# Kernel tuning notes

Hardware: AMD Instinct MI355X
Metric: run time of the kernel (lower is better)

Reference implementation:

```python
import jax, jax.numpy as jnp
import numpy as np

# pywt db4 reconstruction low-pass filter (rec_lo); this is exactly what the
# torch module stores in self.weights (initial_scaling_filter).
DB4_REC_LO = np.array([0.23037781330885523, 0.7148465705525415,
                       0.6308807679295904, -0.02798376941698385,
                       -0.18703481171888114, 0.030841381835986965,
                       0.032883011666982945, -0.010597401784997278],
                      dtype=np.float32)

B, N = 512, 65536  # batch, signal length


def setup_inputs() -> dict:
    key = jax.random.key(0)
    k1, k2, k3 = jax.random.split(key, 3)
    x1 = jax.random.normal(k1, (B, N), dtype=jnp.float32)        # signals
    x2 = jax.random.normal(k2, (B, 1, 8), dtype=jnp.float32)     # coeff placeholder (unused at layer 1)
    x3 = jax.random.normal(k3, (B, 1, 8), dtype=jnp.float32)     # reconstructions placeholder (pass-through)
    weights = jnp.asarray(DB4_REC_LO)                            # rec_lo, the module's Parameter
    return {"x1": x1, "x2": x2, "x3": x3, "weights": weights}


def _dwt_symmetric(x, rec_lo):
    """Batched pywt.dwt(x, 'db4', mode='symmetric'). x: (B, N) -> cA, cD: (B, (N+L-1)//2)."""
    L = rec_lo.shape[0]
    # pywt orthogonal-wavelet filter relations
    dec_lo = rec_lo[::-1]
    sign = jnp.where(jnp.arange(L) % 2 == 0, -1.0, 1.0).astype(rec_lo.dtype)
    dec_hi = sign * rec_lo  # dec_hi[k] = (-1)^(k+1) * rec_lo[k]
    # half-point symmetric extension by L-1 on each side (pywt 'symmetric' mode)
    ext = jnp.pad(x, ((0, 0), (L - 1, L - 1)), mode='symmetric')
    # pywt == np.convolve(ext, dec_f, 'valid')[1::2]; np.convolve flips the
    # filter, so run a correlation with the re-flipped filter, drop the first
    # sample, stride 2.
    ext = ext[:, 1:]
    kern = jnp.stack([dec_lo[::-1], dec_hi[::-1]])[:, None, :]   # (2, 1, L)
    y = jax.lax.conv_general_dilated(ext[:, None, :], kern,
                                     window_strides=(2,), padding='VALID')
    return y[:, 0, :], y[:, 1, :]  # cA, cD


def reference(x1, x2, x3, weights):
    cA, cD = _dwt_symmetric(x1, weights)
    cDs = cD[:, None, :]   # layer_number == 1: cDs = np.array([cD]) per sample
    # layer_number == 1: no IDWT; reconstructions input is returned unchanged
    return (cA, cDs, x3)
```

## Files before the change

kernel.cpp:

```cpp
#include <hip/hip_runtime.h>


__device__ __forceinline__ constexpr float WLc(int t) {
    constexpr float w[8] = {
        0.23037781330885523f,  0.7148465705525415f,  0.6308807679295904f,
       -0.02798376941698385f, -0.18703481171888114f, 0.030841381835986965f,
        0.032883011666982945f,-0.010597401784997278f };
    return w[t];
}
__device__ __forceinline__ constexpr float WHc(int t) {
    return (t & 1) ? -WLc(7 - t) : WLc(7 - t);
}

__global__ __launch_bounds__(256) void dwt_db4_kernel(
    const float* __restrict__ x, float* __restrict__ out,
    int B, int N, int K, int tiles_per_row)
{
    const int blk  = blockIdx.x;
    const int row  = blk / tiles_per_row;
    const int tile = blk - row * tiles_per_row;
    const int trow = tile * 256 + threadIdx.x;
    const int k0   = 2 * trow;
    if (k0 >= K) return;

    const float* __restrict__ xr = x + (long long)row * N;
    const int gbase = 4 * trow - 8;

    float f[12];
    if (gbase >= 0 && gbase + 12 <= N) {
        const float4* __restrict__ s = reinterpret_cast<const float4*>(xr + gbase);
        float4 v0 = s[0], v1 = s[1], v2 = s[2];
        f[0]=v0.x; f[1]=v0.y; f[2]=v0.z; f[3]=v0.w;
        f[4]=v1.x; f[5]=v1.y; f[6]=v1.z; f[7]=v1.w;
        f[8]=v2.x; f[9]=v2.y; f[10]=v2.z; f[11]=v2.w;
    } else {
        #pragma unroll
        for (int m = 0; m < 12; ++m) {
            int g = gbase + m;
            if (g < 0) g = -1 - g;
            if (g >= N) g = 2 * N - 1 - g;
            f[m] = xr[g];
        }
    }

    float a0 = f[2] * WLc(0), d0 = f[2] * WHc(0);
    float a1 = f[4] * WLc(0), d1 = f[4] * WHc(0);
    #pragma unroll
    for (int t = 1; t < 8; ++t) {
        a0 = fmaf(f[2 + t], WLc(t), a0);
        d0 = fmaf(f[2 + t], WHc(t), d0);
        a1 = fmaf(f[4 + t], WLc(t), a1);
        d1 = fmaf(f[4 + t], WHc(t), d1);
    }

    const long long obase = (long long)row * K + k0;
    float* __restrict__ oA = out + obase;
    float* __restrict__ oD = oA + (long long)B * K;

    if (K - k0 >= 2) {
        if ((obase & 1) == 0) {
            *reinterpret_cast<float2*>(oA) = make_float2(a0, a1);
            *reinterpret_cast<float2*>(oD) = make_float2(d0, d1);
        } else {
            oA[0] = a0; oA[1] = a1;
            oD[0] = d0; oD[1] = d1;
        }
    } else {
        oA[0] = a0; oD[0] = d0;
    }
}

__global__ void copy_tail_kernel(const float* __restrict__ src,
                                 float* __restrict__ dst, int n)
{
    int i = blockIdx.x * blockDim.x + threadIdx.x;
    if (i < n) dst[i] = src[i];
}

extern "C" void kernel_launch(void* const* d_in, const int* in_sizes, int n_in,
                              void* d_out, int out_size, void* d_ws, size_t ws_size,
                              hipStream_t stream) {
    const float* x1 = (const float*)d_in[0];
    const float* x3 = (const float*)d_in[2];
    float* out = (float*)d_out;

    const int B = in_sizes[2] / 8;
    const int N = in_sizes[0] / B;
    const int K = (N + 7) / 2;
    const int outs_per_block = 512;
    const int tiles = (K + outs_per_block - 1) / outs_per_block;

    dwt_db4_kernel<<<B * tiles, 256, 0, stream>>>(x1, out, B, N, K, tiles);

    const int n3 = in_sizes[2];
    copy_tail_kernel<<<(n3 + 255) / 256, 256, 0, stream>>>(
        x3, out + 2LL * B * K, n3);
}
```

Baseline: 235.4 us.

## Fuse tail copy, align output stores per row parity, loop tiles per block

Each block now walks 17 consecutive 256-thread tiles instead of one. Output pairs are shifted by row parity so the float2 stores always land on 8-byte alignment; K is odd, so odd rows previously fell back to scalar stores. The x3 pass-through copy is folded into spare threads past the end of each row, which removes the second kernel launch. The cost is fewer blocks, a serial loop inside each block, and more complex boundary handling.

```diff
diff --git a/kernel.cpp b/kernel.cpp
--- a/kernel.cpp
+++ b/kernel.cpp
@@ -13,68 +13,78 @@
 }
 
 __global__ __launch_bounds__(256) void dwt_db4_kernel(
-    const float* __restrict__ x, float* __restrict__ out,
-    int B, int N, int K, int tiles_per_row)
+    const float* __restrict__ x, const float* __restrict__ x3,
+    float* __restrict__ out,
+    int B, int N, int K, int tpr, int tiles_total, int tpb)
 {
-    const int blk  = blockIdx.x;
-    const int row  = blk / tiles_per_row;
-    const int tile = blk - row * tiles_per_row;
-    const int trow = tile * 256 + threadIdx.x;
-    const int k0   = 2 * trow;
-    if (k0 >= K) return;
+    int tile_id = blockIdx.x * tpb;
+    if (tile_id >= tiles_total) return;
+    int row  = tile_id / tpr;
+    int tile = tile_id - row * tpr;
+    const int nit = min(tpb, tiles_total - tile_id);
+    const long long BK = (long long)B * K;
 
-    const float* __restrict__ xr = x + (long long)row * N;
-    const int gbase = 4 * trow - 8;
+    for (int it = 0; it < nit; ++it) {
+        const int trow = (tile << 8) + (int)threadIdx.x;
+        const int s    = row & 1;
+        const int k0   = 2 * trow - s;
 
-    float f[12];
-    if (gbase >= 0 && gbase + 12 <= N) {
-        const float4* __restrict__ s = reinterpret_cast<const float4*>(xr + gbase);
-        float4 v0 = s[0], v1 = s[1], v2 = s[2];
-        f[0]=v0.x; f[1]=v0.y; f[2]=v0.z; f[3]=v0.w;
-        f[4]=v1.x; f[5]=v1.y; f[6]=v1.z; f[7]=v1.w;
-        f[8]=v2.x; f[9]=v2.y; f[10]=v2.z; f[11]=v2.w;
-    } else {
-        #pragma unroll
-        for (int m = 0; m < 12; ++m) {
-            int g = gbase + m;
-            if (g < 0) g = -1 - g;
-            if (g >= N) g = 2 * N - 1 - g;
-            f[m] = xr[g];
+        if (k0 < K) {
+            const float* __restrict__ xr = x + (long long)row * N;
+            const int gbase = 4 * trow - 8;
+
+            float f[12];
+            if (gbase >= 0 && gbase + 12 <= N) {
+                const float4* __restrict__ sp =
+                    reinterpret_cast<const float4*>(xr + gbase);
+                float4 v0 = sp[0], v1 = sp[1], v2 = sp[2];
+                f[0]=v0.x; f[1]=v0.y; f[2]=v0.z; f[3]=v0.w;
+                f[4]=v1.x; f[5]=v1.y; f[6]=v1.z; f[7]=v1.w;
+                f[8]=v2.x; f[9]=v2.y; f[10]=v2.z; f[11]=v2.w;
+            } else {
+                #pragma unroll
+                for (int m = 0; m < 12; ++m) {
+                    int g = gbase + m;
+                    if (g < 0) g = -1 - g;
+                    if (g >= N) g = 2 * N - 1 - g;
+                    f[m] = xr[g];
+                }
+            }
+
+            const int off = 2 - 2 * s;
+            float a0 = f[off]     * WLc(0), d0 = f[off]     * WHc(0);
+            float a1 = f[off + 2] * WLc(0), d1 = f[off + 2] * WHc(0);
+            #pragma unroll
+            for (int t = 1; t < 8; ++t) {
+                a0 = fmaf(f[off + t],     WLc(t), a0);
+                d0 = fmaf(f[off + t],     WHc(t), d0);
+                a1 = fmaf(f[off + 2 + t], WLc(t), a1);
+                d1 = fmaf(f[off + 2 + t], WHc(t), d1);
+            }
+
+            const long long obase = (long long)row * K + k0;
+            float* __restrict__ oA = out + obase;
+            float* __restrict__ oD = oA + BK;
+            const bool v0ok = (k0 >= 0);
+            const bool v1ok = (k0 + 1 < K);
+            if (v0ok && v1ok) {
+                *reinterpret_cast<float2*>(oA) = make_float2(a0, a1);
+                *reinterpret_cast<float2*>(oD) = make_float2(d0, d1);
+            } else if (!v0ok) {
+                oA[1] = a1; oD[1] = d1;
+            } else {
+                oA[0] = a0; oD[0] = d0;
+            }
+        } else {
+            const int j = trow - (K + 1) / 2;
+            if (j >= 0 && j < 8) {
+                out[2 * BK + (long long)row * 8 + j] = x3[(long long)row * 8 + j];
+            }
         }
+
+        ++tile;
+        if (tile == tpr) { tile = 0; ++row; }
     }
-
-    float a0 = f[2] * WLc(0), d0 = f[2] * WHc(0);
-    float a1 = f[4] * WLc(0), d1 = f[4] * WHc(0);
-    #pragma unroll
-    for (int t = 1; t < 8; ++t) {
-        a0 = fmaf(f[2 + t], WLc(t), a0);
-        d0 = fmaf(f[2 + t], WHc(t), d0);
-        a1 = fmaf(f[4 + t], WLc(t), a1);
-        d1 = fmaf(f[4 + t], WHc(t), d1);
-    }
-
-    const long long obase = (long long)row * K + k0;
-    float* __restrict__ oA = out + obase;
-    float* __restrict__ oD = oA + (long long)B * K;
-
-    if (K - k0 >= 2) {
-        if ((obase & 1) == 0) {
-            *reinterpret_cast<float2*>(oA) = make_float2(a0, a1);
-            *reinterpret_cast<float2*>(oD) = make_float2(d0, d1);
-        } else {
-            oA[0] = a0; oA[1] = a1;
-            oD[0] = d0; oD[1] = d1;
-        }
-    } else {
-        oA[0] = a0; oD[0] = d0;
-    }
-}
-
-__global__ void copy_tail_kernel(const float* __restrict__ src,
-                                 float* __restrict__ dst, int n)
-{
-    int i = blockIdx.x * blockDim.x + threadIdx.x;
-    if (i < n) dst[i] = src[i];
 }
 
 extern "C" void kernel_launch(void* const* d_in, const int* in_sizes, int n_in,
@@ -87,12 +97,11 @@
     const int B = in_sizes[2] / 8;
     const int N = in_sizes[0] / B;
     const int K = (N + 7) / 2;
-    const int outs_per_block = 512;
-    const int tiles = (K + outs_per_block - 1) / outs_per_block;
+    const int tpr = ((K + 1) / 2 + 8 + 255) / 256;
+    const int tiles_total = B * tpr;
+    const int tpb = 17;
+    const int grid = (tiles_total + tpb - 1) / tpb;
 
-    dwt_db4_kernel<<<B * tiles, 256, 0, stream>>>(x1, out, B, N, K, tiles);
-
-    const int n3 = in_sizes[2];
-    copy_tail_kernel<<<(n3 + 255) / 256, 256, 0, stream>>>(
-        x3, out + 2LL * B * K, n3);
+    dwt_db4_kernel<<<grid, 256, 0, stream>>>(x1, x3, out, B, N, K,
+                                             tpr, tiles_total, tpb);
 }
```

Result: slower. 254.0 us (+7.9%).

## Process three pair groups per thread with aligned nontemporal float2 stores

Applied to the files above, without the earlier changes.

Each thread now computes three output pairs instead of one and issues all loads up front, using clamped float4 loads for every group and patching the boundary cases afterwards. Output pairs are shifted according to row parity so every float2 store is 8-byte aligned, which removes the scalar-store fallback taken on odd rows. Stores are nontemporal to avoid polluting caches. The cost is more registers per thread and a grid one third the size.

```diff
diff --git a/kernel.cpp b/kernel.cpp
--- a/kernel.cpp
+++ b/kernel.cpp
@@ -1,5 +1,10 @@
 #include <hip/hip_runtime.h>
 
+
+typedef float v2f __attribute__((ext_vector_type(2)));
+
+#define GROUPS 3
+#define PAIRS_PER_BLOCK (GROUPS * 256)
 
 __device__ __forceinline__ constexpr float WLc(int t) {
     constexpr float w[8] = {
@@ -14,59 +19,67 @@
 
 __global__ __launch_bounds__(256) void dwt_db4_kernel(
     const float* __restrict__ x, float* __restrict__ out,
-    int B, int N, int K, int tiles_per_row)
+    int B, int N, int K, int P, int bpr)
 {
-    const int blk  = blockIdx.x;
-    const int row  = blk / tiles_per_row;
-    const int tile = blk - row * tiles_per_row;
-    const int trow = tile * 256 + threadIdx.x;
-    const int k0   = 2 * trow;
-    if (k0 >= K) return;
+    const int blk = blockIdx.x;
+    const int row = blk / bpr;
+    const int tb  = blk - row * bpr;
+    const int tid = threadIdx.x;
+    const int s   = row & 1;
+    const float* __restrict__ xr = x + (long long)row * N;
+    const long long BK = (long long)B * K;
+    const long long rowbase = (long long)row * K;
 
-    const float* __restrict__ xr = x + (long long)row * N;
-    const int gbase = 4 * trow - 8;
-
-    float f[12];
-    if (gbase >= 0 && gbase + 12 <= N) {
-        const float4* __restrict__ s = reinterpret_cast<const float4*>(xr + gbase);
-        float4 v0 = s[0], v1 = s[1], v2 = s[2];
-        f[0]=v0.x; f[1]=v0.y; f[2]=v0.z; f[3]=v0.w;
-        f[4]=v1.x; f[5]=v1.y; f[6]=v1.z; f[7]=v1.w;
-        f[8]=v2.x; f[9]=v2.y; f[10]=v2.z; f[11]=v2.w;
-    } else {
-        #pragma unroll
-        for (int m = 0; m < 12; ++m) {
-            int g = gbase + m;
-            if (g < 0) g = -1 - g;
-            if (g >= N) g = 2 * N - 1 - g;
-            f[m] = xr[g];
-        }
+    int p[GROUPS], gb[GROUPS];
+    float f[GROUPS][12];
+    #pragma unroll
+    for (int g = 0; g < GROUPS; ++g) {
+        p[g]  = tb * PAIRS_PER_BLOCK + (g << 8) + tid;
+        gb[g] = 4 * p[g] - 8;
+        const int cb = min(max(gb[g], 0), N - 12);
+        const float4* sp = reinterpret_cast<const float4*>(xr + cb);
+        float4 v0 = sp[0], v1 = sp[1], v2 = sp[2];
+        f[g][0]=v0.x; f[g][1]=v0.y; f[g][2] =v0.z; f[g][3] =v0.w;
+        f[g][4]=v1.x; f[g][5]=v1.y; f[g][6] =v1.z; f[g][7] =v1.w;
+        f[g][8]=v2.x; f[g][9]=v2.y; f[g][10]=v2.z; f[g][11]=v2.w;
     }
 
-    float a0 = f[2] * WLc(0), d0 = f[2] * WHc(0);
-    float a1 = f[4] * WLc(0), d1 = f[4] * WHc(0);
     #pragma unroll
-    for (int t = 1; t < 8; ++t) {
-        a0 = fmaf(f[2 + t], WLc(t), a0);
-        d0 = fmaf(f[2 + t], WHc(t), d0);
-        a1 = fmaf(f[4 + t], WLc(t), a1);
-        d1 = fmaf(f[4 + t], WHc(t), d1);
-    }
+    for (int g = 0; g < GROUPS; ++g) {
+        if (p[g] >= P) continue;
+        if (gb[g] < 0 || gb[g] > N - 12) {
+            #pragma unroll
+            for (int m = 0; m < 12; ++m) {
+                int q = gb[g] + m;
+                if (q < 0) q = -1 - q;
+                if (q >= N) q = 2 * N - 1 - q;
+                f[g][m] = xr[q];
+            }
+        }
 
-    const long long obase = (long long)row * K + k0;
-    float* __restrict__ oA = out + obase;
-    float* __restrict__ oD = oA + (long long)B * K;
+        const int off = 2 - 2 * s;
+        float a0 = f[g][off]     * WLc(0), d0 = f[g][off]     * WHc(0);
+        float a1 = f[g][off + 2] * WLc(0), d1 = f[g][off + 2] * WHc(0);
+        #pragma unroll
+        for (int t = 1; t < 8; ++t) {
+            a0 = fmaf(f[g][off + t],     WLc(t), a0);
+            d0 = fmaf(f[g][off + t],     WHc(t), d0);
+            a1 = fmaf(f[g][off + 2 + t], WLc(t), a1);
+            d1 = fmaf(f[g][off + 2 + t], WHc(t), d1);
+        }
 
-    if (K - k0 >= 2) {
-        if ((obase & 1) == 0) {
-            *reinterpret_cast<float2*>(oA) = make_float2(a0, a1);
-            *reinterpret_cast<float2*>(oD) = make_float2(d0, d1);
-        } else {
-            oA[0] = a0; oA[1] = a1;
-            oD[0] = d0; oD[1] = d1;
+        const int k0 = 2 * p[g] - s;
+        float* __restrict__ oA = out + rowbase + k0;
+        float* __restrict__ oD = oA + BK;
+        if (k0 >= 0 && k0 + 1 < K) {
+            v2f va = {a0, a1}, vd = {d0, d1};
+            __builtin_nontemporal_store(va, reinterpret_cast<v2f*>(oA));
+            __builtin_nontemporal_store(vd, reinterpret_cast<v2f*>(oD));
+        } else if (k0 < 0) {
+            oA[1] = a1; oD[1] = d1;
+        } else if (k0 < K) {
+            oA[0] = a0; oD[0] = d0;
         }
-    } else {
-        oA[0] = a0; oD[0] = d0;
     }
 }
 
@@ -87,10 +100,11 @@
     const int B = in_sizes[2] / 8;
     const int N = in_sizes[0] / B;
     const int K = (N + 7) / 2;
-    const int outs_per_block = 512;
-    const int tiles = (K + outs_per_block - 1) / outs_per_block;
+    const int P = K / 2 + 1;
+    const int bpr = (P + PAIRS_PER_BLOCK - 1) / PAIRS_PER_BLOCK;
+    const int grid = B * bpr;
 
-    dwt_db4_kernel<<<B * tiles, 256, 0, stream>>>(x1, out, B, N, K, tiles);
+    dwt_db4_kernel<<<grid, 256, 0, stream>>>(x1, out, B, N, K, P, bpr);
 
     const int n3 = in_sizes[2];
     copy_tail_kernel<<<(n3 + 255) / 256, 256, 0, stream>>>(
```

Result: slower. 355.5 us (+51.0%).
